# Kernel tuning notes

Hardware: AMD Instinct MI355X
Metric: run time of the kernel (lower is better)

The kernel has to match this reference:

```python
import jax, jax.numpy as jnp
import numpy as np

EPS = 1e-5

def _c1(W, x, b=None):
    # 1x1 conv on (B,C,J,T)
    y = jnp.einsum('oc,bcjt->bojt', W, x)
    if b is not None:
        y = y + b[None, :, None, None]
    return y

def _c1s(W, x, b=None):
    # 1x1 conv on batch-free (C,J,T)
    y = jnp.einsum('oc,cjt->ojt', W, x)
    if b is not None:
        y = y + b[:, None, None]
    return y

def _bn(x, p):
    # eval-mode batchnorm; p is (4,C) = gamma, beta, running_mean, running_var
    g, b, m, v = p[0], p[1], p[2], p[3]
    shp = (1, -1) + (1,) * (x.ndim - 2)
    inv = g / jnp.sqrt(v + EPS)
    return (x - m.reshape(shp)) * inv.reshape(shp) + b.reshape(shp)

def _adaptive_max_w(x, out_w):
    # AdaptiveMaxPool over last dim of (B,C,W) -> (B,C,out_w), torch bin rule
    W = x.shape[-1]
    cols = []
    for i in range(out_w):
        s = (i * W) // out_w
        e = -((-(i + 1) * W) // out_w)
        cols.append(jnp.max(x[..., s:e], axis=-1))
    return jnp.stack(cols, axis=-1)

def _gcn(x1, g, w, w1, b1, bnp):
    # gcn_spa: y[b,c,j,t] = sum_k g[b,t,j,k] * x1[b,c,k,t]
    y = jnp.einsum('btjk,bckt->bcjt', g, x1)
    out = _c1(w, y) + _c1(w1, x1, b1)
    return jax.nn.relu(_bn(out, bnp))

def setup_inputs() -> dict:
    key = jax.random.key(0)
    B, J, T = 4, 224, 224
    specs = {
        'x': (B, 3, J, T),
        'je1_w': (64, 3), 'je1_b': (64,), 'je2_w': (64, 64), 'je2_b': (64,),
        'se1_w': (64, J), 'se1_b': (64,), 'se2_w': (64, 64), 'se2_b': (64,),
        'te1_w': (64, T), 'te1_b': (64,), 'te2_w': (256, 64), 'te2_b': (256,),
        'g1_w': (256, 128), 'g1_b': (256,), 'g2_w': (256, 128), 'g2_b': (256,),
        'gcn1_w': (128, 128), 'gcn1_w1': (128, 128), 'gcn1_b': (128,),
        'gcn2_w': (256, 128), 'gcn2_w1': (256, 128), 'gcn2_b': (256,),
        'gcn3_w': (256, 256), 'gcn3_w1': (256, 256), 'gcn3_b': (256,),
        'loc1_w': (256, 256, 1, 3), 'loc1_b': (256,),
        'loc2_w': (512, 256), 'loc2_b': (512,),
    }
    bns = {'bn0': 672, 'gcn1_bn': 128, 'gcn2_bn': 256,
           'gcn3_bn': 256, 'loc1_bn': 256, 'loc2_bn': 512}
    out = {}
    for i, (name, shp) in enumerate(specs.items()):
        k = jax.random.fold_in(key, i)
        scale = 1.0 if name == 'x' else 0.1
        out[name] = jax.random.normal(k, shp, dtype=jnp.float32) * scale
    for i, (name, c) in enumerate(bns.items()):
        k = jax.random.fold_in(key, 100 + i)
        out[name] = jax.random.uniform(k, (4, c), dtype=jnp.float32)
    return out

def reference(x, bn0, je1_w, je1_b, je2_w, je2_b, se1_w, se1_b, se2_w, se2_b,
              te1_w, te1_b, te2_w, te2_b, g1_w, g1_b, g2_w, g2_b,
              gcn1_w, gcn1_w1, gcn1_b, gcn1_bn,
              gcn2_w, gcn2_w1, gcn2_b, gcn2_bn,
              gcn3_w, gcn3_w1, gcn3_b, gcn3_bn,
              loc1_w, loc1_b, loc1_bn, loc2_w, loc2_b, loc2_bn):
    bs, c, J, T = x.shape
    eye = jnp.eye(J, dtype=x.dtype)
    # spa one-hot after permute: [c,j,t] = delta_cj; tem: [c,j,t] = delta_ct
    spa_oh = jnp.broadcast_to(eye[:, :, None], (J, J, T))
    tem_oh = jnp.broadcast_to(eye[:, None, :], (T, J, T))
    # embeds of constant one-hots (identical across batch)
    tem1 = jax.nn.relu(_c1s(te2_w, jax.nn.relu(_c1s(te1_w, tem_oh, te1_b)), te2_b))  # (256,J,T)
    spa1 = jax.nn.relu(_c1s(se2_w, jax.nn.relu(_c1s(se1_w, spa_oh, se1_b)), se2_b))  # (64,J,T)
    # joint_embed with norm_data_custom (BN1d over flattened c*J channels)
    xf = _bn(x.reshape(bs, c * J, T), bn0).reshape(bs, c, J, T)
    pos = jax.nn.relu(_c1(je2_w, jax.nn.relu(_c1(je1_w, xf, je1_b)), je2_b))  # (bs,64,J,T)
    h = jnp.concatenate([pos, jnp.broadcast_to(spa1[None], (bs,) + spa1.shape)], axis=1)  # (bs,128,J,T)
    # compute_g_spa: per-timestep joint affinity with softmax
    q = _c1(g1_w, h, g1_b)  # (bs,256,J,T)
    k = _c1(g2_w, h, g2_b)
    g = jax.nn.softmax(jnp.einsum('bcjt,bckt->btjk', q, k), axis=-1)  # (bs,T,J,J)
    h = _gcn(h, g, gcn1_w, gcn1_w1, gcn1_b, gcn1_bn)
    h = _gcn(h, g, gcn2_w, gcn2_w1, gcn2_b, gcn2_bn)
    h = _gcn(h, g, gcn3_w, gcn3_w1, gcn3_b, gcn3_bn)
    h = h + tem1[None]
    # local: AdaptiveMaxPool2d((1,20)) then temporal conv k=(1,3) pad=(0,1)
    h = jnp.max(h, axis=2)           # (bs,256,T)
    h = _adaptive_max_w(h, 20)       # (bs,256,20)
    h = h[:, :, None, :]             # (bs,256,1,20)
    h = jax.lax.conv_general_dilated(h, loc1_w, (1, 1), ((0, 0), (1, 1)),
                                     dimension_numbers=('NCHW', 'OIHW', 'NCHW'))
    h = jax.nn.relu(_bn(h + loc1_b[None, :, None, None], loc1_bn))
    # dropout2d is identity in eval mode
    h = jax.nn.relu(_bn(_c1(loc2_w, h, loc2_b), loc2_bn))
    return jnp.max(h, axis=(2, 3), keepdims=True)  # (bs,512,1,1)
```

## Files before the change

kernel.cpp:

```cpp
#include <hip/hip_runtime.h>
#include <hip/hip_bf16.h>

typedef __hip_bfloat16 bf16;
typedef __attribute__((ext_vector_type(8))) short v8s;
typedef __attribute__((ext_vector_type(4))) float f32x4;
#define EPS 1e-5f
#define MFMA16(a, b, c) __builtin_amdgcn_mfma_f32_16x16x32_bf16(a, b, c, 0, 0, 0)

__device__ __forceinline__ float bfu(unsigned int s) {
  union { unsigned int u; float f; } c; c.u = s << 16; return c.f;
}
__device__ __forceinline__ bf16 f2b(float v) { return __float2bfloat16(v); }

__global__ __launch_bounds__(256) void k_small(
    const float* __restrict__ te1_w, const float* __restrict__ te1_b,
    const float* __restrict__ te2_w, const float* __restrict__ te2_b,
    const float* __restrict__ se1_w, const float* __restrict__ se1_b,
    const float* __restrict__ se2_w, const float* __restrict__ se2_b,
    float* __restrict__ tem1, bf16* __restrict__ spa1T) {
  int idx = blockIdx.x * 256 + threadIdx.x;
  if (idx >= (256 + 64) * 224) return;
  int o = idx / 224, t = idx % 224;
  if (o < 256) {
    float acc = te2_b[o];
    for (int c = 0; c < 64; ++c) {
      float u = fmaxf(te1_w[c * 224 + t] + te1_b[c], 0.f);
      acc += te2_w[o * 64 + c] * u;
    }
    tem1[o * 224 + t] = fmaxf(acc, 0.f);
  } else {
    int oo = o - 256;
    float acc = se2_b[oo];
    for (int c = 0; c < 64; ++c) {
      float u = fmaxf(se1_w[c * 224 + t] + se1_b[c], 0.f);
      acc += se2_w[oo * 64 + c] * u;
    }
    spa1T[t * 64 + oo] = f2b(fmaxf(acc, 0.f));
  }
}

__global__ __launch_bounds__(256) void k_wm(
    const float* __restrict__ g1_w, const float* __restrict__ g2_w,
    const float* __restrict__ g1_b, bf16* __restrict__ WmH, bf16* __restrict__ WmL,
    float* __restrict__ dvec) {
  int idx = blockIdx.x * 256 + threadIdx.x;
  if (idx >= 128 * 128) return;
  int o = idx >> 7, c = idx & 127;
  float acc = 0.f;
  for (int t = 0; t < 256; ++t) acc += g1_w[t * 128 + c] * g2_w[t * 128 + o];
  bf16 hi = f2b(acc);
  WmH[o * 128 + c] = hi;
  WmL[o * 128 + c] = f2b(acc - __bfloat162float(hi));
  if (c == 0) {
    float d = 0.f;
    for (int t = 0; t < 256; ++t) d += g2_w[t * 128 + o] * g1_b[t];
    dvec[o] = d;
  }
}

__global__ __launch_bounds__(256) void k_wcvt(
    const float* __restrict__ g1w, const float* __restrict__ g1w1,
    const float* __restrict__ g2w, const float* __restrict__ g2w1,
    const float* __restrict__ g3w, const float* __restrict__ g3w1,
    const float* __restrict__ je2w, bf16* __restrict__ dst) {
  int idx = blockIdx.x * 256 + threadIdx.x;
  const float* src; size_t base; int off;
  if (idx < 16384)        { src = g1w;  base = 0;      off = idx;          }
  else if (idx < 32768)   { src = g1w1; base = 16384;  off = idx - 16384;  }
  else if (idx < 65536)   { src = g2w;  base = 32768;  off = idx - 32768;  }
  else if (idx < 98304)   { src = g2w1; base = 65536;  off = idx - 65536;  }
  else if (idx < 163840)  { src = g3w;  base = 98304;  off = idx - 98304;  }
  else if (idx < 229376)  { src = g3w1; base = 163840; off = idx - 163840; }
  else if (idx < 233472)  {
    int off2 = idx - 229376;
    float v = je2w[off2];
    bf16 hi = f2b(v);
    dst[229376 + off2] = hi;
    dst[233472 + off2] = f2b(v - __bfloat162float(hi));
    return;
  }
  else return;
  dst[base + off] = f2b(src[off]);
}

__global__ __launch_bounds__(256, 2) void k_h0_mfma(
    const float* __restrict__ x, const float* __restrict__ bn0,
    const float* __restrict__ je1_w, const float* __restrict__ je1_b,
    const bf16* __restrict__ je2wb, const float* __restrict__ je2_b,
    const bf16* __restrict__ spa1T, bf16* __restrict__ H0) {
  __shared__ bf16 Uh[2 * 7168];
  __shared__ bf16 Ul[2 * 7168];
  __shared__ bf16 Wh[2 * 2048];
  __shared__ bf16 Wl[2 * 2048];
  __shared__ float w1s[192], b1s[64];
  const int bt = blockIdx.x;
  const int b = bt / 224, t = bt - b * 224;
  const int tid = threadIdx.x;
  if (tid < 192) w1s[tid] = je1_w[tid];
  if (tid < 64) b1s[tid] = je1_b[tid];
  #pragma unroll
  for (int sh = 0; sh < 2; ++sh) {
    int idx = sh * 256 + tid;
    int kt = idx >> 8, rem = idx & 255;
    int o = rem >> 2, qq = rem & 3;
    v8s wh = *(const v8s*)(je2wb + o * 64 + kt * 32 + qq * 8);
    v8s wl = *(const v8s*)(je2wb + 4096 + o * 64 + kt * 32 + qq * 8);
    *(v8s*)(Wh + kt * 2048 + (o * 4 + qq) * 8) = wh;
    *(v8s*)(Wl + kt * 2048 + (o * 4 + qq) * 8) = wl;
  }
  __syncthreads();
  if (tid < 224) {
    const int j = tid;
    float xf[3];
    #pragma unroll
    for (int c = 0; c < 3; ++c) {
      int ch = c * 224 + j;
      float g = bn0[ch], bb = bn0[672 + ch], m = bn0[1344 + ch], v = bn0[2016 + ch];
      float inv = g * rsqrtf(v + EPS);
      float xv = x[((size_t)(b * 3 + c) * 224 + j) * 224 + t];
      xf[c] = (xv - m) * inv + bb;
    }
    float u[64];
    #pragma unroll
    for (int c = 0; c < 64; ++c) {
      float a = w1s[c * 3] * xf[0] + w1s[c * 3 + 1] * xf[1] + w1s[c * 3 + 2] * xf[2] + b1s[c];
      u[c] = fmaxf(a, 0.f);
    }
    #pragma unroll
    for (int kt = 0; kt < 2; ++kt)
      #pragma unroll
      for (int qq = 0; qq < 4; ++qq) {
        unsigned int ph[4], pl[4];
        #pragma unroll
        for (int e = 0; e < 4; ++e) {
          float v0 = u[kt * 32 + qq * 8 + 2 * e];
          float v1 = u[kt * 32 + qq * 8 + 2 * e + 1];
          bf16 h0 = f2b(v0), h1 = f2b(v1);
          bf16 l0 = f2b(v0 - __bfloat162float(h0));
          bf16 l1 = f2b(v1 - __bfloat162float(h1));
          ph[e] = (unsigned int)__bfloat16_as_ushort(h0) |
                  ((unsigned int)__bfloat16_as_ushort(h1) << 16);
          pl[e] = (unsigned int)__bfloat16_as_ushort(l0) |
                  ((unsigned int)__bfloat16_as_ushort(l1) << 16);
        }
        *(uint4*)(Uh + kt * 7168 + (j * 4 + qq) * 8) = make_uint4(ph[0], ph[1], ph[2], ph[3]);
        *(uint4*)(Ul + kt * 7168 + (j * 4 + qq) * 8) = make_uint4(pl[0], pl[1], pl[2], pl[3]);
      }
    const uint4* sp = (const uint4*)(spa1T + j * 64);
    uint4* dp = (uint4*)(H0 + ((size_t)bt * 224 + j) * 128 + 64);
    #pragma unroll
    for (int i = 0; i < 8; ++i) dp[i] = sp[i];
  }
  __syncthreads();
  const int w = tid >> 6, lane = tid & 63;
  const int l15 = lane & 15, q = lane >> 4;
  for (int mt = w; mt < 14; mt += 4) {
    v8s ah[2], al[2];
    #pragma unroll
    for (int kt = 0; kt < 2; ++kt) {
      ah[kt] = *(const v8s*)(Uh + kt * 7168 + ((mt * 16 + l15) * 4 + q) * 8);
      al[kt] = *(const v8s*)(Ul + kt * 7168 + ((mt * 16 + l15) * 4 + q) * 8);
    }
    #pragma unroll
    for (int nt = 0; nt < 4; ++nt) {
      f32x4 acc = {0.f, 0.f, 0.f, 0.f};
      #pragma unroll
      for (int kt = 0; kt < 2; ++kt) {
        v8s bh = *(const v8s*)(Wh + kt * 2048 + ((nt * 16 + l15) * 4 + q) * 8);
        v8s bl = *(const v8s*)(Wl + kt * 2048 + ((nt * 16 + l15) * 4 + q) * 8);
        acc = MFMA16(ah[kt], bl, acc);
        acc = MFMA16(al[kt], bh, acc);
        acc = MFMA16(ah[kt], bh, acc);
      }
      const int oc = nt * 16 + l15;
      const float bi = je2_b[oc];
      #pragma unroll
      for (int r = 0; r < 4; ++r) {
        size_t m = (size_t)bt * 224 + mt * 16 + q * 4 + r;
        H0[m * 128 + oc] = f2b(fmaxf(acc[r] + bi, 0.f));
      }
    }
  }
}

template <int CIN, int COUT, int DUAL, int WLO, int WRITE_T>
__global__ __launch_bounds__(512, 4) void k_conv_mfma(
    const bf16* __restrict__ in1,
    const bf16* __restrict__ w1h, const bf16* __restrict__ w1l,
    const bf16* __restrict__ in2,
    const bf16* __restrict__ w2h, const bf16* __restrict__ w2l,
    const float* __restrict__ bias, const float* __restrict__ bn,
    int do_relu, bf16* __restrict__ out, bf16* __restrict__ out_t) {
  constexpr int HALF = CIN / 32;
  constexpr int NST = (1 + DUAL) * HALF;
  constexpr int TSZ = 4096;
  constexpr int NT = 2 + WLO;
  __shared__ bf16 smem[2 * NT * TSZ];
  const int tid = threadIdx.x;
  const int w = tid >> 6, lane = tid & 63;
  const int l15 = lane & 15, q = lane >> 4;
  const int mh = w >> 2, nq = w & 3;
  const int m0 = blockIdx.x * 128;
  const int n0blk = blockIdx.y * 128;
  const int n0w = n0blk + nq * 32;
  const int crow = tid >> 2;
  const int ckp = tid & 3;

  f32x4 acc[4][2] = {};
  v8s TA, TH, TL;

  auto gload = [&](int s) {
    const bool second = DUAL && (s >= HALF);
    const bf16* ia = second ? in2 : in1;
    const bf16* wh = second ? w2h : w1h;
    const int kk = (second ? s - HALF : s) * 32 + ckp * 8;
    TA = *(const v8s*)(ia + (size_t)(m0 + crow) * CIN + kk);
    TH = *(const v8s*)(wh + (size_t)(n0blk + crow) * CIN + kk);
    if (WLO) {
      const bf16* wl = second ? w2l : w1l;
      TL = *(const v8s*)(wl + (size_t)(n0blk + crow) * CIN + kk);
    }
  };
  auto swrite = [&](int buf) {
    bf16* b = smem + buf * NT * TSZ;
    *(v8s*)(b + tid * 8) = TA;
    *(v8s*)(b + TSZ + tid * 8) = TH;
    if (WLO) *(v8s*)(b + 2 * TSZ + tid * 8) = TL;
  };

  gload(0);
  swrite(0);
  for (int s = 0; s < NST; ++s) {
    __syncthreads();
    if (s + 1 < NST) gload(s + 1);
    const bf16* base = smem + (s & 1) * NT * TSZ;
    v8s a[4];
    #pragma unroll
    for (int i = 0; i < 4; ++i) {
      const int row = mh * 64 + i * 16 + l15;
      a[i] = *(const v8s*)(base + (row * 4 + q) * 8);
    }
    #pragma unroll
    for (int ns = 0; ns < 2; ++ns) {
      const int ncol = nq * 32 + ns * 16 + l15;
      v8s bh = *(const v8s*)(base + TSZ + (ncol * 4 + q) * 8);
      if (WLO) {
        v8s bl = *(const v8s*)(base + 2 * TSZ + (ncol * 4 + q) * 8);
        #pragma unroll
        for (int i = 0; i < 4; ++i) acc[i][ns] = MFMA16(a[i], bl, acc[i][ns]);
      }
      #pragma unroll
      for (int i = 0; i < 4; ++i) acc[i][ns] = MFMA16(a[i], bh, acc[i][ns]);
    }
    if (s + 1 < NST) swrite((s + 1) & 1);
  }
  #pragma unroll
  for (int ns = 0; ns < 2; ++ns) {
    const int oc = n0w + ns * 16 + l15;
    float sc = 1.f, sh = bias[oc];
    if (bn != nullptr) {
      float g = bn[oc], bb = bn[COUT + oc], m = bn[2 * COUT + oc], v = bn[3 * COUT + oc];
      sc = g * rsqrtf(v + EPS);
      sh = (sh - m) * sc + bb;
    }
    #pragma unroll
    for (int i = 0; i < 4; ++i) {
      const int mbase = m0 + mh * 64 + i * 16 + q * 4;
      float vals[4];
      #pragma unroll
      for (int r = 0; r < 4; ++r) {
        float val = acc[i][ns][r] * sc + sh;
        if (do_relu) val = fmaxf(val, 0.f);
        vals[r] = val;
        out[(size_t)(mbase + r) * COUT + oc] = f2b(val);
      }
      if (WRITE_T) {
        const int bt = mbase / 224;
        const int j = mbase - bt * 224;
        unsigned short s0 = __bfloat16_as_ushort(f2b(vals[0]));
        unsigned short s1 = __bfloat16_as_ushort(f2b(vals[1]));
        unsigned short s2 = __bfloat16_as_ushort(f2b(vals[2]));
        unsigned short s3 = __bfloat16_as_ushort(f2b(vals[3]));
        uint2 pk;
        pk.x = (unsigned int)s0 | ((unsigned int)s1 << 16);
        pk.y = (unsigned int)s2 | ((unsigned int)s3 << 16);
        *(uint2*)((unsigned short*)out_t + ((size_t)bt * COUT + oc) * 224 + j) = pk;
      }
    }
  }
}

__global__ __launch_bounds__(256) void k_transpose128(
    const bf16* __restrict__ src, bf16* __restrict__ dst) {
  const int j0 = blockIdx.x * 32, c0 = blockIdx.y * 32, bt = blockIdx.z;
  __shared__ unsigned short ts[32][33];
  const int tid = threadIdx.x;
  {
    int r = tid >> 3, cg = (tid & 7) * 4;
    const unsigned short* sp =
        (const unsigned short*)src + ((size_t)(bt * 224) + j0 + r) * 128 + c0 + cg;
    uint2 u = *(const uint2*)sp;
    ts[r][cg + 0] = (unsigned short)(u.x & 0xffffu);
    ts[r][cg + 1] = (unsigned short)(u.x >> 16);
    ts[r][cg + 2] = (unsigned short)(u.y & 0xffffu);
    ts[r][cg + 3] = (unsigned short)(u.y >> 16);
  }
  __syncthreads();
  {
    int c = tid >> 3, jg = (tid & 7) * 4;
    uint2 o;
    o.x = (unsigned int)ts[jg + 0][c] | ((unsigned int)ts[jg + 1][c] << 16);
    o.y = (unsigned int)ts[jg + 2][c] | ((unsigned int)ts[jg + 3][c] << 16);
    *(uint2*)((unsigned short*)dst + ((size_t)(bt * 128) + c0 + c) * 224 + j0 + jg) = o;
  }
}

__global__ __launch_bounds__(256, 3) void k_scores_mfma(
    const bf16* __restrict__ A, const bf16* __restrict__ H, bf16* __restrict__ G) {
  const int bid = blockIdx.x;
  const int xcd = bid & 7, slot = bid >> 3;
  const int mtg = slot & 3, bt = (slot >> 2) * 8 + xcd;
  const int w = threadIdx.x >> 6, lane = threadIdx.x & 63;
  const int mt = mtg * 4 + w;
  if (mt >= 14) return;
  const int l15 = lane & 15, q = lane >> 4;
  const int j0 = mt * 16;
  const bf16* Ab = A + (size_t)bt * 224 * 128;
  const bf16* Hb = H + (size_t)bt * 224 * 128;
  v8s a[4];
  #pragma unroll
  for (int ks = 0; ks < 4; ++ks)
    a[ks] = *(const v8s*)(Ab + (size_t)(j0 + l15) * 128 + ks * 32 + q * 8);
  f32x4 s[14];
  #pragma unroll
  for (int nt = 0; nt < 14; ++nt) {
    f32x4 acc = {0.f, 0.f, 0.f, 0.f};
    #pragma unroll
    for (int ks = 0; ks < 4; ++ks) {
      v8s b = *(const v8s*)(Hb + (size_t)(nt * 16 + l15) * 128 + ks * 32 + q * 8);
      acc = MFMA16(a[ks], b, acc);
    }
    s[nt] = acc;
  }
  bf16* Gb = G + ((size_t)bt * 224 + j0) * 224;
  #pragma unroll
  for (int r = 0; r < 4; ++r) {
    float mx = -1e30f;
    #pragma unroll
    for (int nt = 0; nt < 14; ++nt) mx = fmaxf(mx, s[nt][r]);
    mx = fmaxf(mx, __shfl_xor(mx, 1));
    mx = fmaxf(mx, __shfl_xor(mx, 2));
    mx = fmaxf(mx, __shfl_xor(mx, 4));
    mx = fmaxf(mx, __shfl_xor(mx, 8));
    float sum = 0.f;
    #pragma unroll
    for (int nt = 0; nt < 14; ++nt) {
      float e = __expf(s[nt][r] - mx);
      s[nt][r] = e;
      sum += e;
    }
    sum += __shfl_xor(sum, 1);
    sum += __shfl_xor(sum, 2);
    sum += __shfl_xor(sum, 4);
    sum += __shfl_xor(sum, 8);
    const float inv = 1.f / sum;
    const int jr = q * 4 + r;
    #pragma unroll
    for (int nt = 0; nt < 14; ++nt)
      Gb[(size_t)jr * 224 + nt * 16 + l15] = f2b(s[nt][r] * inv);
  }
}

template <int C>
__global__ __launch_bounds__(256, 2) void k_apply_mfma(
    const bf16* __restrict__ G, const bf16* __restrict__ Ht,
    bf16* __restrict__ Y) {
  constexpr int NST = C / 64;
  __shared__ bf16 Gs[7168];
  __shared__ bf16 Ht2[2 * 14336];
  const int bid = blockIdx.x;
  const int xcd = bid & 7, slot = bid >> 3;
  const int jt = slot % 7, bt = (slot / 7) * 8 + xcd;
  const int tid = threadIdx.x;
  const int w = tid >> 6, lane = tid & 63;
  const int l15 = lane & 15, q = lane >> 4;
  const int j0 = jt * 32;
  const bf16* Gb = G + (size_t)bt * 224 * 224;
  const bf16* Hb = Ht + (size_t)bt * C * 224;
  bf16* Yb = Y + (size_t)bt * 224 * C;
  #pragma unroll
  for (int it = 0; it < 4; ++it) {
    int c = it * 256 + tid;
    if (c < 896)
      *(v8s*)(Gs + c * 8) = *(const v8s*)(Gb + (size_t)j0 * 224 + c * 8);
  }
  v8s T[7];
  auto gload = [&](int g) {
    #pragma unroll
    for (int it = 0; it < 7; ++it) {
      int c = it * 256 + tid;
      T[it] = *(const v8s*)(Hb + (size_t)g * 64 * 224 + c * 8);
    }
  };
  auto swrite = [&](int buf) {
    bf16* bp = Ht2 + buf * 14336;
    #pragma unroll
    for (int it = 0; it < 7; ++it) {
      int c = it * 256 + tid;
      *(v8s*)(bp + c * 8) = T[it];
    }
  };
  gload(0);
  swrite(0);
  __syncthreads();
  v8s a0[7], a1[7];
  #pragma unroll
  for (int ks = 0; ks < 7; ++ks) {
    a0[ks] = *(const v8s*)(Gs + ((size_t)l15 * 28 + ks * 4 + q) * 8);
    a1[ks] = *(const v8s*)(Gs + ((size_t)(16 + l15) * 28 + ks * 4 + q) * 8);
  }
  for (int g = 0; g < NST; ++g) {
    if (g) __syncthreads();
    if (g + 1 < NST) gload(g + 1);
    const bf16* bp = Ht2 + (g & 1) * 14336;
    f32x4 acc0 = {0.f, 0.f, 0.f, 0.f};
    f32x4 acc1 = {0.f, 0.f, 0.f, 0.f};
    #pragma unroll
    for (int ks = 0; ks < 7; ++ks) {
      v8s b = *(const v8s*)(bp + ((size_t)(w * 16 + l15) * 28 + ks * 4 + q) * 8);
      acc0 = MFMA16(a0[ks], b, acc0);
      acc1 = MFMA16(a1[ks], b, acc1);
    }
    const int c = g * 64 + w * 16 + l15;
    #pragma unroll
    for (int r = 0; r < 4; ++r) {
      Yb[(size_t)(j0 + q * 4 + r) * C + c] = f2b(acc0[r]);
      Yb[(size_t)(j0 + 16 + q * 4 + r) * C + c] = f2b(acc1[r]);
    }
    if (g + 1 < NST) swrite((g + 1) & 1);
  }
}

__global__ __launch_bounds__(256) void k_reduce(
    const bf16* __restrict__ H3, float* __restrict__ Hred, int row0) {
  int t = blockIdx.x;
  int jb = blockIdx.y;
  int o = threadIdx.x;
  const unsigned short* p =
      (const unsigned short*)(H3 + ((size_t)t * 224 + jb * 32) * 256 + o);
  float mx = 0.f;
  #pragma unroll 8
  for (int j = 0; j < 32; ++j) mx = fmaxf(mx, bfu(p[(size_t)j * 256]));
  atomicMax((unsigned int*)&Hred[(size_t)(row0 + t) * 256 + o], __float_as_uint(mx));
}

__global__ __launch_bounds__(256) void k_head_a(
    const float* __restrict__ Hred, const float* __restrict__ tem1,
    float* __restrict__ Hm) {
  int b = blockIdx.x, i = blockIdx.y, c = threadIdx.x;
  int s = (i * 224) / 20, e = ((i + 1) * 224 + 19) / 20;
  float mx = -1e30f;
  for (int t = s; t < e; ++t)
    mx = fmaxf(mx, Hred[((size_t)b * 224 + t) * 256 + c] + tem1[c * 224 + t]);
  Hm[((size_t)b * 20 + i) * 256 + c] = mx;
}

__global__ __launch_bounds__(256) void k_head_b(
    const float* __restrict__ Hm, const float* __restrict__ loc1_w,
    const float* __restrict__ loc1_b, const float* __restrict__ loc1_bn,
    float* __restrict__ Z1) {
  int b = blockIdx.x, r = blockIdx.y;
  __shared__ float hs[3 * 256];
  int tid = threadIdx.x;
  for (int idx = tid; idx < 768; idx += 256) {
    int dx = idx >> 8, c = idx & 255;
    int u = r + dx - 1;
    hs[idx] = (u >= 0 && u < 20) ? Hm[((size_t)b * 20 + u) * 256 + c] : 0.f;
  }
  __syncthreads();
  int o = tid;
  float acc = loc1_b[o];
  const float* wp = loc1_w + (size_t)o * 768;
  #pragma unroll 4
  for (int c = 0; c < 256; ++c) {
    acc += wp[c * 3 + 0] * hs[c] + wp[c * 3 + 1] * hs[256 + c] + wp[c * 3 + 2] * hs[512 + c];
  }
  float g = loc1_bn[o], bb = loc1_bn[256 + o], m = loc1_bn[512 + o], v = loc1_bn[768 + o];
  float sc = g * rsqrtf(v + EPS);
  Z1[((size_t)b * 20 + r) * 256 + o] = fmaxf((acc - m) * sc + bb, 0.f);
}

__global__ __launch_bounds__(512) void k_head_c(
    const float* __restrict__ Z1, const float* __restrict__ loc2_w,
    const float* __restrict__ loc2_b, const float* __restrict__ loc2_bn,
    float* __restrict__ out) {
  int b = blockIdx.x;
  int tid = threadIdx.x;
  __shared__ float zs[20 * 256];
  for (int idx = tid; idx < 5120; idx += 512) zs[idx] = Z1[(size_t)b * 5120 + idx];
  __syncthreads();
  int o2 = tid;
  float acc[20];
  float bi = loc2_b[o2];
  #pragma unroll
  for (int r = 0; r < 20; ++r) acc[r] = bi;
  const float* wp = loc2_w + (size_t)o2 * 256;
  for (int c = 0; c < 256; ++c) {
    float wv = wp[c];
    #pragma unroll
    for (int r = 0; r < 20; ++r) acc[r] += wv * zs[r * 256 + c];
  }
  float g = loc2_bn[o2], bb = loc2_bn[512 + o2], m = loc2_bn[1024 + o2], v = loc2_bn[1536 + o2];
  float sc = g * rsqrtf(v + EPS);
  float best = -1e30f;
  #pragma unroll
  for (int r = 0; r < 20; ++r) best = fmaxf(best, fmaxf((acc[r] - m) * sc + bb, 0.f));
  out[(size_t)b * 512 + o2] = best;
}

extern "C" void kernel_launch(void* const* d_in, const int* in_sizes, int n_in,
                              void* d_out, int out_size, void* d_ws, size_t ws_size,
                              hipStream_t stream) {
  const float* x       = (const float*)d_in[0];
  const float* je1_w   = (const float*)d_in[1];
  const float* je1_b   = (const float*)d_in[2];
  const float* je2_w   = (const float*)d_in[3];
  const float* je2_b   = (const float*)d_in[4];
  const float* se1_w   = (const float*)d_in[5];
  const float* se1_b   = (const float*)d_in[6];
  const float* se2_w   = (const float*)d_in[7];
  const float* se2_b   = (const float*)d_in[8];
  const float* te1_w   = (const float*)d_in[9];
  const float* te1_b   = (const float*)d_in[10];
  const float* te2_w   = (const float*)d_in[11];
  const float* te2_b   = (const float*)d_in[12];
  const float* g1_w    = (const float*)d_in[13];
  const float* g1_b    = (const float*)d_in[14];
  const float* g2_w    = (const float*)d_in[15];
  const float* gcn1_w  = (const float*)d_in[17];
  const float* gcn1_w1 = (const float*)d_in[18];
  const float* gcn1_b  = (const float*)d_in[19];
  const float* gcn2_w  = (const float*)d_in[20];
  const float* gcn2_w1 = (const float*)d_in[21];
  const float* gcn2_b  = (const float*)d_in[22];
  const float* gcn3_w  = (const float*)d_in[23];
  const float* gcn3_w1 = (const float*)d_in[24];
  const float* gcn3_b  = (const float*)d_in[25];
  const float* loc1_w  = (const float*)d_in[26];
  const float* loc1_b  = (const float*)d_in[27];
  const float* loc2_w  = (const float*)d_in[28];
  const float* loc2_b  = (const float*)d_in[29];
  const float* bn0     = (const float*)d_in[30];
  const float* gcn1_bn = (const float*)d_in[31];
  const float* gcn2_bn = (const float*)d_in[32];
  const float* gcn3_bn = (const float*)d_in[33];
  const float* loc1_bn = (const float*)d_in[34];
  const float* loc2_bn = (const float*)d_in[35];
  float* out = (float*)d_out;
  (void)in_sizes; (void)n_in; (void)out_size; (void)ws_size;

  char* ws = (char*)d_ws;
  size_t off = 0;
  auto take = [&](size_t bytes) -> char* {
    char* p = ws + off;
    off += (bytes + 255) & ~(size_t)255;
    return p;
  };
  const size_t M  = 200704;
  const size_t Mc = 50176;
  float* tem1  = (float*)take(256 * 224 * 4);
  bf16* spa1T  = (bf16*)take(224 * 64 * 2);
  bf16* WmH    = (bf16*)take(128 * 128 * 2);
  bf16* WmL    = (bf16*)take(128 * 128 * 2);
  float* dvec  = (float*)take(128 * 4);
  bf16* wb     = (bf16*)take(237568 * 2);
  float* Hm    = (float*)take(4 * 20 * 256 * 4);
  float* Z1    = (float*)take(4 * 20 * 256 * 4);
  float* Hred  = (float*)take(896 * 256 * 4);
  bf16* H0    = (bf16*)take(M * 128 * 2);
  bf16* Afull = (bf16*)take(M * 128 * 2);
  bf16* YZ  = (bf16*)take(Mc * 256 * 2);
  bf16* Wb  = (bf16*)take(Mc * 256 * 2);
  bf16* HtV = (bf16*)take(Mc * 256 * 2);
  bf16* Gm  = (bf16*)take(Mc * 224 * 2);
  bf16* Yr = YZ;
  bf16* Zr = YZ + Mc * 128;

  bf16* g1w_h  = wb;
  bf16* g1w1_h = wb + 16384;
  bf16* g2w_h  = wb + 32768;
  bf16* g2w1_h = wb + 65536;
  bf16* g3w_h  = wb + 98304;
  bf16* g3w1_h = wb + 163840;
  bf16* je2wb  = wb + 229376;

  hipMemsetAsync(Hred, 0, 896 * 256 * 4, stream);
  k_small<<<280, 256, 0, stream>>>(te1_w, te1_b, te2_w, te2_b,
                                   se1_w, se1_b, se2_w, se2_b, tem1, spa1T);
  k_wm<<<64, 256, 0, stream>>>(g1_w, g2_w, g1_b, WmH, WmL, dvec);
  k_wcvt<<<912, 256, 0, stream>>>(gcn1_w, gcn1_w1, gcn2_w, gcn2_w1,
                                  gcn3_w, gcn3_w1, je2_w, wb);
  k_h0_mfma<<<896, 256, 0, stream>>>(x, bn0, je1_w, je1_b, je2wb, je2_b, spa1T, H0);

  k_conv_mfma<128, 128, 0, 1, 0><<<dim3(1568, 1), 512, 0, stream>>>(
      H0, WmH, WmL, nullptr, nullptr, nullptr, dvec, nullptr, 0, Afull, nullptr);

  for (int b = 0; b < 4; ++b) {
    const bf16* H0c = H0 + (size_t)b * Mc * 128;
    const bf16* Ac  = Afull + (size_t)b * Mc * 128;
    k_transpose128<<<dim3(7, 4, 224), 256, 0, stream>>>(H0c, HtV);
    k_scores_mfma<<<896, 256, 0, stream>>>(Ac, H0c, Gm);
    k_apply_mfma<128><<<1568, 256, 0, stream>>>(Gm, HtV, Yr);
    k_conv_mfma<128, 128, 1, 0, 1><<<dim3(392, 1), 512, 0, stream>>>(
        Yr, g1w_h, nullptr, H0c, g1w1_h, nullptr, gcn1_b, gcn1_bn, 1, Zr, HtV);
    k_apply_mfma<128><<<1568, 256, 0, stream>>>(Gm, HtV, Yr);
    k_conv_mfma<128, 256, 1, 0, 1><<<dim3(392, 2), 512, 0, stream>>>(
        Yr, g2w_h, nullptr, Zr, g2w1_h, nullptr, gcn2_b, gcn2_bn, 1, Wb, HtV);
    k_apply_mfma<256><<<1568, 256, 0, stream>>>(Gm, HtV, YZ);
    k_conv_mfma<256, 256, 1, 0, 0><<<dim3(392, 2), 512, 0, stream>>>(
        YZ, g3w_h, nullptr, Wb, g3w1_h, nullptr, gcn3_b, gcn3_bn, 1, HtV, nullptr);
    k_reduce<<<dim3(224, 7), 256, 0, stream>>>(HtV, Hred, b * 224);
  }
  k_head_a<<<dim3(4, 20), 256, 0, stream>>>(Hred, tem1, Hm);
  k_head_b<<<dim3(4, 20), 256, 0, stream>>>(Hm, loc1_w, loc1_b, loc1_bn, Z1);
  k_head_c<<<4, 512, 0, stream>>>(Z1, loc2_w, loc2_b, loc2_bn, out);
}
```

Measured before the change: 932.6 us.

## Fuse H0 transpose into embedding kernel and joint max-reduce into gcn3 epilogue

The embedding kernel now also writes a transposed copy of H0, with the broadcast spa1 half copied from a pre-transposed buffer, so the per-batch transpose kernel is removed. The last gcn conv no longer writes its 256-channel output. It instead reduces each 4-row group to a max and applies it to Hred with atomicMax, which removes the separate reduce kernel and its full read of H3. The trade-offs are more atomics inside the conv epilogue and an extra M×128 transposed buffer written up front.

```diff
diff --git a/kernel.cpp b/kernel.cpp
--- a/kernel.cpp
+++ b/kernel.cpp
@@ -17,7 +17,7 @@
     const float* __restrict__ te2_w, const float* __restrict__ te2_b,
     const float* __restrict__ se1_w, const float* __restrict__ se1_b,
     const float* __restrict__ se2_w, const float* __restrict__ se2_b,
-    float* __restrict__ tem1, bf16* __restrict__ spa1T) {
+    float* __restrict__ tem1, bf16* __restrict__ spa1T, bf16* __restrict__ spa1O) {
   int idx = blockIdx.x * 256 + threadIdx.x;
   if (idx >= (256 + 64) * 224) return;
   int o = idx / 224, t = idx % 224;
@@ -35,7 +35,9 @@
       float u = fmaxf(se1_w[c * 224 + t] + se1_b[c], 0.f);
       acc += se2_w[oo * 64 + c] * u;
     }
-    spa1T[t * 64 + oo] = f2b(fmaxf(acc, 0.f));
+    bf16 v = f2b(fmaxf(acc, 0.f));
+    spa1T[t * 64 + oo] = v;
+    spa1O[oo * 224 + t] = v;
   }
 }
 
@@ -87,7 +89,8 @@
     const float* __restrict__ x, const float* __restrict__ bn0,
     const float* __restrict__ je1_w, const float* __restrict__ je1_b,
     const bf16* __restrict__ je2wb, const float* __restrict__ je2_b,
-    const bf16* __restrict__ spa1T, bf16* __restrict__ H0) {
+    const bf16* __restrict__ spa1T, const bf16* __restrict__ spa1O,
+    bf16* __restrict__ H0, bf16* __restrict__ H0t) {
   __shared__ bf16 Uh[2 * 7168];
   __shared__ bf16 Ul[2 * 7168];
   __shared__ bf16 Wh[2 * 2048];
@@ -107,6 +110,11 @@
     v8s wl = *(const v8s*)(je2wb + 4096 + o * 64 + kt * 32 + qq * 8);
     *(v8s*)(Wh + kt * 2048 + (o * 4 + qq) * 8) = wh;
     *(v8s*)(Wl + kt * 2048 + (o * 4 + qq) * 8) = wl;
+  }
+  for (int idx = tid; idx < 3584; idx += 256) {
+    int o = idx / 56, jc = idx % 56;
+    *(uint2*)((unsigned short*)H0t + ((size_t)bt * 128 + 64 + o) * 224 + jc * 4) =
+        *(const uint2*)((const unsigned short*)spa1O + o * 224 + jc * 4);
   }
   __syncthreads();
   if (tid < 224) {
@@ -174,23 +182,31 @@
       }
       const int oc = nt * 16 + l15;
       const float bi = je2_b[oc];
+      unsigned short s4[4];
       #pragma unroll
       for (int r = 0; r < 4; ++r) {
         size_t m = (size_t)bt * 224 + mt * 16 + q * 4 + r;
-        H0[m * 128 + oc] = f2b(fmaxf(acc[r] + bi, 0.f));
+        bf16 bv = f2b(fmaxf(acc[r] + bi, 0.f));
+        s4[r] = __bfloat16_as_ushort(bv);
+        H0[m * 128 + oc] = bv;
       }
-    }
-  }
-}
-
-template <int CIN, int COUT, int DUAL, int WLO, int WRITE_T>
+      uint2 pk;
+      pk.x = (unsigned int)s4[0] | ((unsigned int)s4[1] << 16);
+      pk.y = (unsigned int)s4[2] | ((unsigned int)s4[3] << 16);
+      *(uint2*)((unsigned short*)H0t + ((size_t)bt * 128 + oc) * 224 + mt * 16 + q * 4) = pk;
+    }
+  }
+}
+
+template <int CIN, int COUT, int DUAL, int WLO, int WRITE_T, int REDMAX>
 __global__ __launch_bounds__(512, 4) void k_conv_mfma(
     const bf16* __restrict__ in1,
     const bf16* __restrict__ w1h, const bf16* __restrict__ w1l,
     const bf16* __restrict__ in2,
     const bf16* __restrict__ w2h, const bf16* __restrict__ w2l,
     const float* __restrict__ bias, const float* __restrict__ bn,
-    int do_relu, bf16* __restrict__ out, bf16* __restrict__ out_t) {
+    int do_relu, bf16* __restrict__ out, bf16* __restrict__ out_t,
+    float* __restrict__ hred) {
   constexpr int HALF = CIN / 32;
   constexpr int NST = (1 + DUAL) * HALF;
   constexpr int TSZ = 4096;
@@ -272,7 +288,12 @@
         float val = acc[i][ns][r] * sc + sh;
         if (do_relu) val = fmaxf(val, 0.f);
         vals[r] = val;
-        out[(size_t)(mbase + r) * COUT + oc] = f2b(val);
+        if (!REDMAX) out[(size_t)(mbase + r) * COUT + oc] = f2b(val);
+      }
+      if (REDMAX) {
+        const int t = mbase / 224;
+        float mx = fmaxf(fmaxf(vals[0], vals[1]), fmaxf(vals[2], vals[3]));
+        atomicMax((unsigned int*)&hred[(size_t)t * COUT + oc], __float_as_uint(mx));
       }
       if (WRITE_T) {
         const int bt = mbase / 224;
@@ -287,31 +308,6 @@
         *(uint2*)((unsigned short*)out_t + ((size_t)bt * COUT + oc) * 224 + j) = pk;
       }
     }
-  }
-}
-
-__global__ __launch_bounds__(256) void k_transpose128(
-    const bf16* __restrict__ src, bf16* __restrict__ dst) {
-  const int j0 = blockIdx.x * 32, c0 = blockIdx.y * 32, bt = blockIdx.z;
-  __shared__ unsigned short ts[32][33];
-  const int tid = threadIdx.x;
-  {
-    int r = tid >> 3, cg = (tid & 7) * 4;
-    const unsigned short* sp =
-        (const unsigned short*)src + ((size_t)(bt * 224) + j0 + r) * 128 + c0 + cg;
-    uint2 u = *(const uint2*)sp;
-    ts[r][cg + 0] = (unsigned short)(u.x & 0xffffu);
-    ts[r][cg + 1] = (unsigned short)(u.x >> 16);
-    ts[r][cg + 2] = (unsigned short)(u.y & 0xffffu);
-    ts[r][cg + 3] = (unsigned short)(u.y >> 16);
-  }
-  __syncthreads();
-  {
-    int c = tid >> 3, jg = (tid & 7) * 4;
-    uint2 o;
-    o.x = (unsigned int)ts[jg + 0][c] | ((unsigned int)ts[jg + 1][c] << 16);
-    o.y = (unsigned int)ts[jg + 2][c] | ((unsigned int)ts[jg + 3][c] << 16);
-    *(uint2*)((unsigned short*)dst + ((size_t)(bt * 128) + c0 + c) * 224 + j0 + jg) = o;
   }
 }
 
@@ -439,19 +435,6 @@
     }
     if (g + 1 < NST) swrite((g + 1) & 1);
   }
-}
-
-__global__ __launch_bounds__(256) void k_reduce(
-    const bf16* __restrict__ H3, float* __restrict__ Hred, int row0) {
-  int t = blockIdx.x;
-  int jb = blockIdx.y;
-  int o = threadIdx.x;
-  const unsigned short* p =
-      (const unsigned short*)(H3 + ((size_t)t * 224 + jb * 32) * 256 + o);
-  float mx = 0.f;
-  #pragma unroll 8
-  for (int j = 0; j < 32; ++j) mx = fmaxf(mx, bfu(p[(size_t)j * 256]));
-  atomicMax((unsigned int*)&Hred[(size_t)(row0 + t) * 256 + o], __float_as_uint(mx));
 }
 
 __global__ __launch_bounds__(256) void k_head_a(
@@ -570,6 +553,7 @@
   const size_t Mc = 50176;
   float* tem1  = (float*)take(256 * 224 * 4);
   bf16* spa1T  = (bf16*)take(224 * 64 * 2);
+  bf16* spa1O  = (bf16*)take(64 * 224 * 2);
   bf16* WmH    = (bf16*)take(128 * 128 * 2);
   bf16* WmL    = (bf16*)take(128 * 128 * 2);
   float* dvec  = (float*)take(128 * 4);
@@ -578,6 +562,7 @@
   float* Z1    = (float*)take(4 * 20 * 256 * 4);
   float* Hred  = (float*)take(896 * 256 * 4);
   bf16* H0    = (bf16*)take(M * 128 * 2);
+  bf16* Ht0   = (bf16*)take(M * 128 * 2);
   bf16* Afull = (bf16*)take(M * 128 * 2);
   bf16* YZ  = (bf16*)take(Mc * 256 * 2);
   bf16* Wb  = (bf16*)take(Mc * 256 * 2);
@@ -596,30 +581,31 @@
 
   hipMemsetAsync(Hred, 0, 896 * 256 * 4, stream);
   k_small<<<280, 256, 0, stream>>>(te1_w, te1_b, te2_w, te2_b,
-                                   se1_w, se1_b, se2_w, se2_b, tem1, spa1T);
+                                   se1_w, se1_b, se2_w, se2_b, tem1, spa1T, spa1O);
   k_wm<<<64, 256, 0, stream>>>(g1_w, g2_w, g1_b, WmH, WmL, dvec);
   k_wcvt<<<912, 256, 0, stream>>>(gcn1_w, gcn1_w1, gcn2_w, gcn2_w1,
                                   gcn3_w, gcn3_w1, je2_w, wb);
-  k_h0_mfma<<<896, 256, 0, stream>>>(x, bn0, je1_w, je1_b, je2wb, je2_b, spa1T, H0);
-
-  k_conv_mfma<128, 128, 0, 1, 0><<<dim3(1568, 1), 512, 0, stream>>>(
-      H0, WmH, WmL, nullptr, nullptr, nullptr, dvec, nullptr, 0, Afull, nullptr);
+  k_h0_mfma<<<896, 256, 0, stream>>>(x, bn0, je1_w, je1_b, je2wb, je2_b,
+                                     spa1T, spa1O, H0, Ht0);
+
+  k_conv_mfma<128, 128, 0, 1, 0, 0><<<dim3(1568, 1), 512, 0, stream>>>(
+      H0, WmH, WmL, nullptr, nullptr, nullptr, dvec, nullptr, 0, Afull, nullptr, nullptr);
 
   for (int b = 0; b < 4; ++b) {
-    const bf16* H0c = H0 + (size_t)b * Mc * 128;
-    const bf16* Ac  = Afull + (size_t)b * Mc * 128;
-    k_transpose128<<<dim3(7, 4, 224), 256, 0, stream>>>(H0c, HtV);
+    const bf16* H0c  = H0 + (size_t)b * Mc * 128;
+    const bf16* H0tc = Ht0 + (size_t)b * Mc * 128;
+    const bf16* Ac   = Afull + (size_t)b * Mc * 128;
     k_scores_mfma<<<896, 256, 0, stream>>>(Ac, H0c, Gm);
+    k_apply_mfma<128><<<1568, 256, 0, stream>>>(Gm, H0tc, Yr);
+    k_conv_mfma<128, 128, 1, 0, 1, 0><<<dim3(392, 1), 512, 0, stream>>>(
+        Yr, g1w_h, nullptr, H0c, g1w1_h, nullptr, gcn1_b, gcn1_bn, 1, Zr, HtV, nullptr);
     k_apply_mfma<128><<<1568, 256, 0, stream>>>(Gm, HtV, Yr);
-    k_conv_mfma<128, 128, 1, 0, 1><<<dim3(392, 1), 512, 0, stream>>>(
-        Yr, g1w_h, nullptr, H0c, g1w1_h, nullptr, gcn1_b, gcn1_bn, 1, Zr, HtV);
-    k_apply_mfma<128><<<1568, 256, 0, stream>>>(Gm, HtV, Yr);
-    k_conv_mfma<128, 256, 1, 0, 1><<<dim3(392, 2), 512, 0, stream>>>(
-        Yr, g2w_h, nullptr, Zr, g2w1_h, nullptr, gcn2_b, gcn2_bn, 1, Wb, HtV);
+    k_conv_mfma<128, 256, 1, 0, 1, 0><<<dim3(392, 2), 512, 0, stream>>>(
+        Yr, g2w_h, nullptr, Zr, g2w1_h, nullptr, gcn2_b, gcn2_bn, 1, Wb, HtV, nullptr);
     k_apply_mfma<256><<<1568, 256, 0, stream>>>(Gm, HtV, YZ);
-    k_conv_mfma<256, 256, 1, 0, 0><<<dim3(392, 2), 512, 0, stream>>>(
-        YZ, g3w_h, nullptr, Wb, g3w1_h, nullptr, gcn3_b, gcn3_bn, 1, HtV, nullptr);
-    k_reduce<<<dim3(224, 7), 256, 0, stream>>>(HtV, Hred, b * 224);
+    k_conv_mfma<256, 256, 1, 0, 0, 1><<<dim3(392, 2), 512, 0, stream>>>(
+        YZ, g3w_h, nullptr, Wb, g3w1_h, nullptr, gcn3_b, gcn3_bn, 1, nullptr, nullptr,
+        Hred + (size_t)b * 224 * 256);
   }
   k_head_a<<<dim3(4, 20), 256, 0, stream>>>(Hred, tem1, Hm);
   k_head_b<<<dim3(4, 20), 256, 0, stream>>>(Hm, loc1_w, loc1_b, loc1_bn, Z1);
```

Result: slower. 986.5 us (+5.8%).
